# Performance work log

Hardware: AMD Instinct MI355X
Metric: run time of the kernel (lower is better)

The kernel has to match this reference:

```python
import jax, jax.numpy as jnp
import numpy as np
import math

D_MODEL = 512
NHEAD = 8
N_LAYERS = 3
D_FF = 2048
INPUT_DIM = 128
NUM_CLASSES = 64
FACTOR = 5


def setup_inputs() -> dict:
    key = jax.random.key(0)
    ks = jax.random.split(key, 24)
    s = 0.02
    d, f, nl = D_MODEL, D_FF, N_LAYERS
    inp = {
        "x": jax.random.normal(ks[0], (4, 1024, INPUT_DIM), dtype=jnp.float32),
        "W_emb": jax.random.normal(ks[1], (INPUT_DIM, d), dtype=jnp.float32) * s,
        "b_emb": jnp.zeros((d,), jnp.float32),
        "Wq": jax.random.normal(ks[2], (nl, d, d), dtype=jnp.float32) * s,
        "bq": jnp.zeros((nl, d), jnp.float32),
        "Wk": jax.random.normal(ks[3], (nl, d, d), dtype=jnp.float32) * s,
        "bk": jnp.zeros((nl, d), jnp.float32),
        "Wv": jax.random.normal(ks[4], (nl, d, d), dtype=jnp.float32) * s,
        "bv": jnp.zeros((nl, d), jnp.float32),
        "Wo": jax.random.normal(ks[5], (nl, d, d), dtype=jnp.float32) * s,
        "bo": jnp.zeros((nl, d), jnp.float32),
        "ln1_g": jnp.ones((nl, d), jnp.float32),
        "ln1_b": jnp.zeros((nl, d), jnp.float32),
        "W1": jax.random.normal(ks[6], (nl, d, f), dtype=jnp.float32) * s,
        "b1": jnp.zeros((nl, f), jnp.float32),
        "W2": jax.random.normal(ks[7], (nl, f, d), dtype=jnp.float32) * s,
        "b2": jnp.zeros((nl, d), jnp.float32),
        "ln2_g": jnp.ones((nl, d), jnp.float32),
        "ln2_b": jnp.zeros((nl, d), jnp.float32),
        "W_dec": jax.random.normal(ks[8], (d, NUM_CLASSES), dtype=jnp.float32) * s,
        "b_dec": jnp.zeros((NUM_CLASSES,), jnp.float32),
    }
    return inp


def _layer_norm(x, g, b, eps=1e-5):
    m = jnp.mean(x, axis=-1, keepdims=True)
    v = jnp.var(x, axis=-1, keepdims=True)
    return (x - m) * jax.lax.rsqrt(v + eps) * g + b


def _pos_encoding(L, d):
    pos = jnp.arange(L, dtype=jnp.float32)[:, None]
    div = jnp.exp(jnp.arange(0, d, 2, dtype=jnp.float32) * (-math.log(10000.0) / d))
    pe = jnp.zeros((L, d), jnp.float32)
    pe = pe.at[:, 0::2].set(jnp.sin(pos * div))
    pe = pe.at[:, 1::2].set(jnp.cos(pos * div))
    return pe


def _prob_sparse_attn(x, Wq, bq, Wk, bk, Wv, bv, Wo, bo):
    B, L, d = x.shape
    H, dk = NHEAD, d // NHEAD
    u = min(L, int(FACTOR * math.log(L)) if L > 1 else L)
    Q = (x @ Wq + bq).reshape(B, L, H, dk).transpose(0, 2, 1, 3)  # bhld
    K = (x @ Wk + bk).reshape(B, L, H, dk).transpose(0, 2, 1, 3)
    V = (x @ Wv + bv).reshape(B, L, H, dk).transpose(0, 2, 1, 3)
    scores = jnp.einsum("bhld,bhmd->bhlm", Q, K) / math.sqrt(dk)  # [B,H,L,L]
    kth = jax.lax.top_k(scores, u)[0][..., -1:]  # kth-largest per row
    scores = jnp.where(scores < kth, -10000.0, scores)
    attn = jax.nn.softmax(scores, axis=-1)
    out = jnp.einsum("bhlm,bhmd->bhld", attn, V)
    out = out.transpose(0, 2, 1, 3).reshape(B, L, d)
    return out @ Wo + bo


def reference(x, W_emb, b_emb, Wq, bq, Wk, bk, Wv, bv, Wo, bo,
              ln1_g, ln1_b, W1, b1, W2, b2, ln2_g, ln2_b, W_dec, b_dec):
    B, L, _ = x.shape
    h = (x @ W_emb + b_emb) * math.sqrt(D_MODEL)
    h = h + _pos_encoding(L, D_MODEL)[None]
    for i in range(N_LAYERS):
        a = _prob_sparse_attn(h, Wq[i], bq[i], Wk[i], bk[i], Wv[i], bv[i], Wo[i], bo[i])
        h = _layer_norm(h + a, ln1_g[i], ln1_b[i])
        ff = jax.nn.relu(h @ W1[i] + b1[i]) @ W2[i] + b2[i]
        h = _layer_norm(h + ff, ln2_g[i], ln2_b[i])
    return h @ W_dec + b_dec
```

## Files before the change

kernel.cpp:

```cpp
#include <hip/hip_runtime.h>
#include <math.h>

#define SEQ 1024
#define BATCH 4
#define DMODEL 512
#define NHEAD 8
#define DK 64
#define DFF 2048
#define U_TOP 34
#define ROWS (BATCH * SEQ)

typedef unsigned short ushort_t;
typedef __attribute__((ext_vector_type(8))) short short8;
typedef __attribute__((ext_vector_type(4))) float float4v;

__device__ inline ushort_t f2bf(float f) {
  unsigned u = __float_as_uint(f);
  unsigned r = u + 0x7fffu + ((u >> 16) & 1u);
  return (ushort_t)(r >> 16);
}
__device__ inline float bf2f(ushort_t u) {
  return __uint_as_float((unsigned)u << 16);
}
__device__ inline float keyinv(unsigned cand) {
  unsigned fb = (cand & 0x80000000u) ? (cand ^ 0x80000000u) : ~cand;
  return __uint_as_float(fb);
}

union H16 { _Float16 h; unsigned short u; };
__device__ inline unsigned short h2u(float f) {
  H16 t; t.h = (_Float16)f; return t.u;
}
__device__ inline float u2h(unsigned short u) {
  H16 t; t.u = u; return (float)t.h;
}
__device__ inline int mbcnt64(unsigned long long m) {
  int lo = __builtin_amdgcn_mbcnt_lo((unsigned)m, 0);
  return __builtin_amdgcn_mbcnt_hi((unsigned)(m >> 32), lo);
}

__device__ inline void glds16(const void* g, void* l) {
  __builtin_amdgcn_global_load_lds(
      (const __attribute__((address_space(1))) unsigned int*)g,
      (__attribute__((address_space(3))) unsigned int*)l, 16, 0, 0);
}

__device__ inline void bitonic64x2(float& a, float& b, int lane) {
#pragma unroll
  for (int k = 2; k <= 64; k <<= 1) {
#pragma unroll
    for (int j = k >> 1; j > 0; j >>= 1) {
      float pa = __shfl_xor(a, j);
      float pb = __shfl_xor(b, j);
      bool keepMin = (((lane & k) != 0) == ((lane & j) == 0));
      a = keepMin ? fminf(a, pa) : fmaxf(a, pa);
      b = keepMin ? fminf(b, pb) : fmaxf(b, pb);
    }
  }
}

template <int RELU, int SPLIT>
__global__ __launch_bounds__(256) void gemm128(
    const ushort_t* __restrict__ A, const short* __restrict__ Bt,
    const float* __restrict__ b0, const float* __restrict__ b1,
    const float* __restrict__ b2, ushort_t* __restrict__ Cout,
    int K, int N, int zCstride) {
  __shared__ short As[128 * 32];
  __shared__ short Bs[128 * 32];

  const int tid = threadIdx.x;
  const int lane = tid & 63, w = tid >> 6;
  const int wm = w >> 1, wn = w & 1;
  const int quad = lane >> 4, r16 = lane & 15;
  const int bm = blockIdx.y * 128, bn = blockIdx.x * 128;

  const int srow = lane >> 2, skseg = lane & 3;
  const ushort_t* Ag0 = A + (size_t)(bm + w * 16 + srow) * K + skseg * 8;
  const ushort_t* Ag1 = Ag0 + (size_t)64 * K;
  const short* Bg0 = Bt + (size_t)(bn + w * 16 + srow) * K + skseg * 8;
  const short* Bg1 = Bg0 + (size_t)64 * K;
  short* lA0 = As + (w * 16) * 32;
  short* lA1 = As + (64 + w * 16) * 32;
  short* lB0 = Bs + (w * 16) * 32;
  short* lB1 = Bs + (64 + w * 16) * 32;

  float4v acc[4][4];
#pragma unroll
  for (int m = 0; m < 4; ++m)
#pragma unroll
    for (int n = 0; n < 4; ++n) acc[m][n] = (float4v){0.f, 0.f, 0.f, 0.f};

  for (int k0 = 0; k0 < K; k0 += 32) {
    __syncthreads();
    glds16(Ag0 + k0, lA0);
    glds16(Ag1 + k0, lA1);
    glds16(Bg0 + k0, lB0);
    glds16(Bg1 + k0, lB1);
    __syncthreads();

    short8 af[4], bfr[4];
#pragma unroll
    for (int m = 0; m < 4; ++m)
      af[m] = *(const short8*)&As[(wm * 64 + m * 16 + r16) * 32 + quad * 8];
#pragma unroll
    for (int n = 0; n < 4; ++n)
      bfr[n] = *(const short8*)&Bs[(wn * 64 + n * 16 + r16) * 32 + quad * 8];
#pragma unroll
    for (int m = 0; m < 4; ++m)
#pragma unroll
      for (int n = 0; n < 4; ++n)
        acc[m][n] = __builtin_amdgcn_mfma_f32_16x16x32_bf16(af[m], bfr[n],
                                                            acc[m][n], 0, 0, 0);
  }

  const int z = SPLIT ? (bn >> 9) : 0;
  const float* bias = (z == 0) ? b0 : (z == 1 ? b1 : b2);
  const int cbase = SPLIT ? (bn & 511) : bn;
  const int strideN = SPLIT ? 512 : N;
  ushort_t* C = Cout + (SPLIT ? (size_t)z * zCstride : (size_t)0);

  float bias_n[4];
#pragma unroll
  for (int n = 0; n < 4; ++n)
    bias_n[n] = bias[cbase + wn * 64 + n * 16 + r16];

#pragma unroll
  for (int m = 0; m < 4; ++m) {
#pragma unroll
    for (int n = 0; n < 4; ++n) {
      int col = cbase + wn * 64 + n * 16 + r16;
#pragma unroll
      for (int reg = 0; reg < 4; ++reg) {
        int row = bm + wm * 64 + m * 16 + quad * 4 + reg;
        float v = acc[m][n][reg] + bias_n[n];
        if (RELU) v = fmaxf(v, 0.f);
        C[(size_t)row * strideN + col] = f2bf(v);
      }
    }
  }
}

__global__ __launch_bounds__(256) void gemm128sk(
    const ushort_t* __restrict__ A, const short* __restrict__ Bt,
    const float* __restrict__ bias, ushort_t* __restrict__ pout,
    int K, int Ks) {
  __shared__ short As[128 * 32];
  __shared__ short Bs[128 * 32];

  const int tid = threadIdx.x;
  const int lane = tid & 63, w = tid >> 6;
  const int wm = w >> 1, wn = w & 1;
  const int quad = lane >> 4, r16 = lane & 15;
  const int bm = blockIdx.y * 128, bn = blockIdx.x * 128;
  const int z = blockIdx.z;
  const int koff = z * Ks;

  const int srow = lane >> 2, skseg = lane & 3;
  const ushort_t* Ag0 =
      A + (size_t)(bm + w * 16 + srow) * K + skseg * 8 + koff;
  const ushort_t* Ag1 = Ag0 + (size_t)64 * K;
  const short* Bg0 = Bt + (size_t)(bn + w * 16 + srow) * K + skseg * 8 + koff;
  const short* Bg1 = Bg0 + (size_t)64 * K;
  short* lA0 = As + (w * 16) * 32;
  short* lA1 = As + (64 + w * 16) * 32;
  short* lB0 = Bs + (w * 16) * 32;
  short* lB1 = Bs + (64 + w * 16) * 32;

  float4v acc[4][4];
#pragma unroll
  for (int m = 0; m < 4; ++m)
#pragma unroll
    for (int n = 0; n < 4; ++n) acc[m][n] = (float4v){0.f, 0.f, 0.f, 0.f};

  for (int k0 = 0; k0 < Ks; k0 += 32) {
    __syncthreads();
    glds16(Ag0 + k0, lA0);
    glds16(Ag1 + k0, lA1);
    glds16(Bg0 + k0, lB0);
    glds16(Bg1 + k0, lB1);
    __syncthreads();

    short8 af[4], bfr[4];
#pragma unroll
    for (int m = 0; m < 4; ++m)
      af[m] = *(const short8*)&As[(wm * 64 + m * 16 + r16) * 32 + quad * 8];
#pragma unroll
    for (int n = 0; n < 4; ++n)
      bfr[n] = *(const short8*)&Bs[(wn * 64 + n * 16 + r16) * 32 + quad * 8];
#pragma unroll
    for (int m = 0; m < 4; ++m)
#pragma unroll
      for (int n = 0; n < 4; ++n)
        acc[m][n] = __builtin_amdgcn_mfma_f32_16x16x32_bf16(af[m], bfr[n],
                                                            acc[m][n], 0, 0, 0);
  }

  ushort_t* P = pout + (size_t)z * 2097152;
  float bias_n[4];
#pragma unroll
  for (int n = 0; n < 4; ++n)
    bias_n[n] = (z == 0) ? bias[bn + wn * 64 + n * 16 + r16] : 0.f;

#pragma unroll
  for (int m = 0; m < 4; ++m) {
#pragma unroll
    for (int n = 0; n < 4; ++n) {
      int col = bn + wn * 64 + n * 16 + r16;
#pragma unroll
      for (int reg = 0; reg < 4; ++reg) {
        int row = bm + wm * 64 + m * 16 + quad * 4 + reg;
        float v = acc[m][n][reg] + bias_n[n];
        P[(size_t)row * 512 + col] = f2bf(v);
      }
    }
  }
}

template <int RELU, int OUTBF16, int EPI, int ADDC>
__global__ __launch_bounds__(256) void gemm64(
    const ushort_t* __restrict__ A, const short* __restrict__ Bt,
    const float* __restrict__ bias, void* __restrict__ Cout,
    const ushort_t* __restrict__ Cadd, int K, int N) {
  __shared__ short As[64 * 32];
  __shared__ short Bs[64 * 32];

  const int tid = threadIdx.x;
  const int lane = tid & 63, w = tid >> 6;
  const int wm = w >> 1, wn = w & 1;
  const int quad = lane >> 4, r16 = lane & 15;
  const int bm = blockIdx.y * 64, bn = blockIdx.x * 64;

  const int srow = tid >> 2, skseg = tid & 3;
  const ushort_t* Ag = A + (size_t)(bm + srow) * K + skseg * 8;
  const short* Bg = Bt + (size_t)(bn + srow) * K + skseg * 8;
  short* lA = As + w * 512;
  short* lB = Bs + w * 512;

  float4v acc[2][2];
#pragma unroll
  for (int m = 0; m < 2; ++m)
#pragma unroll
    for (int n = 0; n < 2; ++n) acc[m][n] = (float4v){0.f, 0.f, 0.f, 0.f};

  for (int k0 = 0; k0 < K; k0 += 32) {
    __syncthreads();
    glds16(Ag + k0, lA);
    glds16(Bg + k0, lB);
    __syncthreads();

    short8 af[2], bfr[2];
#pragma unroll
    for (int m = 0; m < 2; ++m)
      af[m] = *(const short8*)&As[(wm * 32 + m * 16 + r16) * 32 + quad * 8];
#pragma unroll
    for (int n = 0; n < 2; ++n)
      bfr[n] = *(const short8*)&Bs[(wn * 32 + n * 16 + r16) * 32 + quad * 8];
#pragma unroll
    for (int m = 0; m < 2; ++m)
#pragma unroll
      for (int n = 0; n < 2; ++n)
        acc[m][n] = __builtin_amdgcn_mfma_f32_16x16x32_bf16(af[m], bfr[n],
                                                            acc[m][n], 0, 0, 0);
  }

  const float pe_c = (float)(-9.210340371976184 / 512.0);
  const float sqrtd = 22.62741699796952f;

  float bias_n[2];
#pragma unroll
  for (int n = 0; n < 2; ++n) bias_n[n] = bias[bn + wn * 32 + n * 16 + r16];

#pragma unroll
  for (int m = 0; m < 2; ++m) {
#pragma unroll
    for (int n = 0; n < 2; ++n) {
      int col = bn + wn * 32 + n * 16 + r16;
#pragma unroll
      for (int reg = 0; reg < 4; ++reg) {
        int row = bm + wm * 32 + m * 16 + quad * 4 + reg;
        float v = acc[m][n][reg] + bias_n[n];
        if (RELU) v = fmaxf(v, 0.f);
        if (EPI == 2) {
          int pos = row & (SEQ - 1);
          float e = __expf((float)(col & ~1) * pe_c);
          float arg = (float)pos * e;
          v = v * sqrtd + ((col & 1) ? __cosf(arg) : __sinf(arg));
        }
        if (ADDC) v += bf2f(Cadd[(size_t)row * N + col]);
        if (OUTBF16) {
          ((ushort_t*)Cout)[(size_t)row * N + col] = f2bf(v);
        } else {
          ((float*)Cout)[(size_t)row * N + col] = v;
        }
      }
    }
  }
}

__global__ __launch_bounds__(256) void convert_all(
    const float* __restrict__ Wq, const float* __restrict__ Wk,
    const float* __restrict__ Wv, const float* __restrict__ Wo,
    const float* __restrict__ W1, const float* __restrict__ W2,
    const float* __restrict__ W_emb, const float* __restrict__ W_dec,
    short* __restrict__ wt) {
  __shared__ float t[32][33];
  int id = blockIdx.x;
  const float* src;
  short* dst;
  int K, N, tk, tn;
  if (id < 9216) {
    int lay = id / 3072, r = id % 3072;
    short* wl = wt + (size_t)lay * 3145728;
    const size_t wsz = 512 * 512;
    if (r < 1024) {
      int wi = r >> 8, tile = r & 255;
      const float* base = (wi == 0) ? Wq : (wi == 1) ? Wk : (wi == 2) ? Wv : Wo;
      src = base + lay * wsz;
      dst = wl + wi * 262144;
      K = 512; N = 512; tk = tile >> 4; tn = tile & 15;
    } else if (r < 2048) {
      int tile = r - 1024;
      src = W1 + (size_t)lay * 512 * 2048;
      dst = wl + 1048576;
      K = 512; N = 2048; tk = tile >> 6; tn = tile & 63;
    } else {
      int tile = r - 2048;
      src = W2 + (size_t)lay * 2048 * 512;
      dst = wl + 2097152;
      K = 2048; N = 512; tk = tile >> 4; tn = tile & 15;
    }
  } else {
    int r = id - 9216;
    if (r < 64) {
      src = W_emb; dst = wt + 9437184; K = 128; N = 512; tk = r >> 4; tn = r & 15;
    } else {
      r -= 64;
      src = W_dec; dst = wt + 9502720; K = 512; N = 64; tk = r >> 1; tn = r & 1;
    }
  }
  const int k0 = tk * 32, n0 = tn * 32;
  const int tx = threadIdx.x, ty = threadIdx.y;
#pragma unroll
  for (int i = 0; i < 4; ++i) {
    int r = ty + i * 8;
    t[r][tx] = src[(size_t)(k0 + r) * N + n0 + tx];
  }
  __syncthreads();
#pragma unroll
  for (int i = 0; i < 4; ++i) {
    int r = ty + i * 8;
    dst[(size_t)(n0 + r) * K + k0 + tx] = (short)f2bf(t[tx][r]);
  }
}

__global__ __launch_bounds__(256) void f32_to_bf16_kernel(
    const float* __restrict__ src, ushort_t* __restrict__ dst) {
  int i = blockIdx.x * blockDim.x + threadIdx.x;
  float4 v = ((const float4*)src)[i];
  ushort4 o;
  o.x = f2bf(v.x); o.y = f2bf(v.y); o.z = f2bf(v.z); o.w = f2bf(v.w);
  ((ushort4*)dst)[i] = o;
}

__global__ __launch_bounds__(256) void ln_red_kernel(
    const ushort_t* __restrict__ pa, const ushort_t* __restrict__ pb,
    const float* __restrict__ g, const float* __restrict__ bb,
    ushort_t* __restrict__ hb) {
  const int row = blockIdx.x * 4 + (threadIdx.x >> 6);
  const int lane = threadIdx.x & 63;
  const size_t base = (size_t)row * DMODEL + lane * 8;
  uint4 ra = *(const uint4*)(pa + base);
  uint4 rb = *(const uint4*)(pb + base);
  uint4 rh = *(const uint4*)(hb + base);
  unsigned aa[4] = {ra.x, ra.y, ra.z, ra.w};
  unsigned ab[4] = {rb.x, rb.y, rb.z, rb.w};
  unsigned ah[4] = {rh.x, rh.y, rh.z, rh.w};
  float v[8];
#pragma unroll
  for (int k = 0; k < 4; ++k) {
    v[2 * k] = bf2f((ushort_t)(aa[k] & 0xffff)) +
               bf2f((ushort_t)(ab[k] & 0xffff)) +
               bf2f((ushort_t)(ah[k] & 0xffff));
    v[2 * k + 1] = bf2f((ushort_t)(aa[k] >> 16)) +
                   bf2f((ushort_t)(ab[k] >> 16)) +
                   bf2f((ushort_t)(ah[k] >> 16));
  }
  float sum = 0.f, sq = 0.f;
#pragma unroll
  for (int k = 0; k < 8; ++k) { sum += v[k]; sq += v[k] * v[k]; }
#pragma unroll
  for (int off = 32; off; off >>= 1) {
    sum += __shfl_xor(sum, off);
    sq += __shfl_xor(sq, off);
  }
  float mean = sum * (1.f / 512.f);
  float var = fmaxf(sq * (1.f / 512.f) - mean * mean, 0.f);
  float rstd = 1.f / sqrtf(var + 1e-5f);
  float4 g0 = *(const float4*)(g + lane * 8);
  float4 g1 = *(const float4*)(g + lane * 8 + 4);
  float4 c0 = *(const float4*)(bb + lane * 8);
  float4 c1 = *(const float4*)(bb + lane * 8 + 4);
  float gg[8] = {g0.x, g0.y, g0.z, g0.w, g1.x, g1.y, g1.z, g1.w};
  float cc[8] = {c0.x, c0.y, c0.z, c0.w, c1.x, c1.y, c1.z, c1.w};
  uint4 out;
  unsigned* op = (unsigned*)&out;
#pragma unroll
  for (int k = 0; k < 4; ++k) {
    float y0 = (v[2 * k] - mean) * rstd * gg[2 * k] + cc[2 * k];
    float y1 = (v[2 * k + 1] - mean) * rstd * gg[2 * k + 1] + cc[2 * k + 1];
    op[k] = (unsigned)f2bf(y0) | ((unsigned)f2bf(y1) << 16);
  }
  *(uint4*)(hb + base) = out;
}

#define SST 1048

__global__ __launch_bounds__(512, 8) void attn_kernel(
    const ushort_t* __restrict__ Qb, const ushort_t* __restrict__ Kb,
    const ushort_t* __restrict__ Vb, ushort_t* __restrict__ Ob) {
  __shared__ _Float16 s16[16 * SST];
  __shared__ unsigned plist[16][64];

  const int tid = threadIdx.x;
  const int q0 = blockIdx.x * 16;
  const int h = blockIdx.y;
  const int b = blockIdx.z;
  const int w = tid >> 6;
  const int lane = tid & 63;
  const int quad = lane >> 4, r16 = lane & 15;

  {
    const int j0 = w * 128;
    const ushort_t* qrow =
        Qb + (size_t)(b * SEQ + q0 + r16) * DMODEL + h * DK + quad * 8;
    short8 aq0 = *(const short8*)qrow;
    short8 aq1 = *(const short8*)(qrow + 32);

#pragma unroll
    for (int nt = 0; nt < 8; ++nt) {
      const ushort_t* krow =
          Kb + (size_t)(b * SEQ + j0 + nt * 16 + r16) * DMODEL + h * DK +
          quad * 8;
      short8 bk0 = *(const short8*)krow;
      short8 bk1 = *(const short8*)(krow + 32);
      float4v a = (float4v){0.f, 0.f, 0.f, 0.f};
      a = __builtin_amdgcn_mfma_f32_16x16x32_bf16(aq0, bk0, a, 0, 0, 0);
      a = __builtin_amdgcn_mfma_f32_16x16x32_bf16(aq1, bk1, a, 0, 0, 0);
#pragma unroll
      for (int reg = 0; reg < 4; ++reg)
        s16[(quad * 4 + reg) * SST + j0 + nt * 16 + r16] =
            (_Float16)(a[reg] * 0.125f);
    }
  }
  __syncthreads();

  {
    const int qa = w, qb2 = w + 8;
    const _Float16* sa = &s16[qa * SST];
    const _Float16* sb = &s16[qb2 * SST];

    float la = -1e30f, lb = -1e30f;
#pragma unroll
    for (int i = 0; i < 16; ++i) {
      la = fmaxf(la, (float)sa[lane + 64 * i]);
      lb = fmaxf(lb, (float)sb[lane + 64 * i]);
    }

    float sva = la, svb = lb;
    bitonic64x2(sva, svb, lane);
    const float mxa = __shfl(sva, 0), mxb = __shfl(svb, 0);
    const float fTa = __shfl(sva, 33), fTb = __shfl(svb, 33);

    int ca = 0, cb = 0;
#pragma unroll
    for (int i = 0; i < 16; ++i) {
      float va = (float)sa[lane + 64 * i];
      float vb = (float)sb[lane + 64 * i];
      bool ka = va >= fTa, kb = vb >= fTb;
      unsigned long long ma = __ballot(ka);
      unsigned long long mb = __ballot(kb);
      if (ka) {
        int p = ca + mbcnt64(ma);
        if (p < 64)
          plist[qa][p] = ((unsigned)(lane + 64 * i) << 16) |
                         h2u(__expf(va - mxa));
      }
      if (kb) {
        int p = cb + mbcnt64(mb);
        if (p < 64)
          plist[qb2][p] = ((unsigned)(lane + 64 * i) << 16) |
                          h2u(__expf(vb - mxb));
      }
      ca += (int)__popcll(ma);
      cb += (int)__popcll(mb);
    }

    if (__builtin_expect(ca > 64, 0)) {
      unsigned ans = 0u;
      int cge = ca;
      bool ex = false;
      for (int bit = 31; bit >= 0 && cge > 64 && !ex; --bit) {
        unsigned cand = ans | (1u << bit);
        float fc = keyinv(cand);
        int c = 0;
#pragma unroll
        for (int i = 0; i < 16; ++i)
          c += (int)__popcll(__ballot((float)sa[lane + 64 * i] >= fc));
        if (c >= U_TOP) { ans = cand; cge = c; ex = (c == U_TOP); }
      }
      float fa2 = keyinv(ans);
      int cc = 0;
#pragma unroll
      for (int i = 0; i < 16; ++i) {
        float va = (float)sa[lane + 64 * i];
        bool ka = va >= fa2;
        unsigned long long ma = __ballot(ka);
        if (ka) {
          int p = cc + mbcnt64(ma);
          if (p < 64)
            plist[qa][p] = ((unsigned)(lane + 64 * i) << 16) |
                           h2u(__expf(va - mxa));
        }
        cc += (int)__popcll(ma);
      }
      ca = cc;
    }
    if (__builtin_expect(cb > 64, 0)) {
      unsigned ans = 0u;
      int cge = cb;
      bool ex = false;
      for (int bit = 31; bit >= 0 && cge > 64 && !ex; --bit) {
        unsigned cand = ans | (1u << bit);
        float fc = keyinv(cand);
        int c = 0;
#pragma unroll
        for (int i = 0; i < 16; ++i)
          c += (int)__popcll(__ballot((float)sb[lane + 64 * i] >= fc));
        if (c >= U_TOP) { ans = cand; cge = c; ex = (c == U_TOP); }
      }
      float fb2 = keyinv(ans);
      int cc = 0;
#pragma unroll
      for (int i = 0; i < 16; ++i) {
        float vb = (float)sb[lane + 64 * i];
        bool kb = vb >= fb2;
        unsigned long long mb = __ballot(kb);
        if (kb) {
          int p = cc + mbcnt64(mb);
          if (p < 64)
            plist[qb2][p] = ((unsigned)(lane + 64 * i) << 16) |
                            h2u(__expf(vb - mxb));
        }
        cc += (int)__popcll(mb);
      }
      cb = cc;
    }
    ca = ca > 64 ? 64 : ca;
    cb = cb > 64 ? 64 : cb;

    unsigned pua = (lane < ca) ? plist[qa][lane] : 0u;
    unsigned pub = (lane < cb) ? plist[qb2][lane] : 0u;
    float ea = u2h((unsigned short)(pua & 0xffffu));
    float eb = u2h((unsigned short)(pub & 0xffffu));

    float s2a = ea, s2b = eb;
    bitonic64x2(s2a, s2b, lane);
    const float tha = __shfl(s2a, 33), thb = __shfl(s2b, 33);

    bool keepa = ea >= tha, keepb = eb >= thb;
    unsigned long long kma = __ballot(keepa);
    unsigned long long kmb = __ballot(keepb);
    int na = (int)__popcll(kma), nb = (int)__popcll(kmb);
    float za = keepa ? ea : 0.f, zb = keepb ? eb : 0.f;
#pragma unroll
    for (int off = 32; off; off >>= 1) {
      za += __shfl_xor(za, off);
      zb += __shfl_xor(zb, off);
    }
    int posa = mbcnt64(kma), posb = mbcnt64(kmb);
    if (keepa) plist[qa][posa] = pua;
    if (keepb) plist[qb2][posb] = pub;

    const ushort_t* vbase = Vb + (size_t)b * SEQ * DMODEL + h * DK;
    float oa = 0.f, ob = 0.f;
    int nmax = na > nb ? na : nb;
    for (int i = 0; i < nmax; i += 2) {
      unsigned ua0 = (i < na) ? plist[qa][i] : 0u;
      unsigned ua1 = (i + 1 < na) ? plist[qa][i + 1] : 0u;
      unsigned ub0 = (i < nb) ? plist[qb2][i] : 0u;
      unsigned ub1 = (i + 1 < nb) ? plist[qb2][i + 1] : 0u;
      float pa0 = bf2f(vbase[(size_t)(ua0 >> 16) * DMODEL + lane]);
      float pa1 = bf2f(vbase[(size_t)(ua1 >> 16) * DMODEL + lane]);
      float pb0 = bf2f(vbase[(size_t)(ub0 >> 16) * DMODEL + lane]);
      float pb1 = bf2f(vbase[(size_t)(ub1 >> 16) * DMODEL + lane]);
      oa += u2h((unsigned short)(ua0 & 0xffffu)) * pa0 +
            u2h((unsigned short)(ua1 & 0xffffu)) * pa1;
      ob += u2h((unsigned short)(ub0 & 0xffffu)) * pb0 +
            u2h((unsigned short)(ub1 & 0xffffu)) * pb1;
    }
    oa /= za;
    ob /= zb;
    Ob[(size_t)(b * SEQ + q0 + qa) * DMODEL + h * DK + lane] = f2bf(oa);
    Ob[(size_t)(b * SEQ + q0 + qb2) * DMODEL + h * DK + lane] = f2bf(ob);
  }
}

extern "C" void kernel_launch(void* const* d_in, const int* in_sizes, int n_in,
                              void* d_out, int out_size, void* d_ws,
                              size_t ws_size, hipStream_t stream) {
  const float* x = (const float*)d_in[0];
  const float* W_emb = (const float*)d_in[1];
  const float* b_emb = (const float*)d_in[2];
  const float* Wq = (const float*)d_in[3];
  const float* bq = (const float*)d_in[4];
  const float* Wk = (const float*)d_in[5];
  const float* bk = (const float*)d_in[6];
  const float* Wv = (const float*)d_in[7];
  const float* bv = (const float*)d_in[8];
  const float* Wo = (const float*)d_in[9];
  const float* bo = (const float*)d_in[10];
  const float* ln1_g = (const float*)d_in[11];
  const float* ln1_b = (const float*)d_in[12];
  const float* W1 = (const float*)d_in[13];
  const float* b1 = (const float*)d_in[14];
  const float* W2 = (const float*)d_in[15];
  const float* b2 = (const float*)d_in[16];
  const float* ln2_g = (const float*)d_in[17];
  const float* ln2_b = (const float*)d_in[18];
  const float* W_dec = (const float*)d_in[19];
  const float* b_dec = (const float*)d_in[20];

  char* wsb = (char*)d_ws;
  ushort_t* qkv = (ushort_t*)wsb;
  ushort_t* ffh = (ushort_t*)wsb;
  ushort_t* wop = (ushort_t*)wsb;
  ushort_t* ao = (ushort_t*)(wsb + ((size_t)16 << 20));
  ushort_t* xb = (ushort_t*)(wsb + ((size_t)16 << 20));
  ushort_t* ffp = (ushort_t*)(wsb + ((size_t)16 << 20));
  ushort_t* hb = (ushort_t*)(wsb + ((size_t)24 << 20));
  short* wt = (short*)(wsb + ((size_t)28 << 20));
  short* wembT = wt + 9437184;
  short* wdecT = wt + 9502720;

  f32_to_bf16_kernel<<<dim3(512), 256, 0, stream>>>(x, xb);
  convert_all<<<dim3(9312), dim3(32, 8), 0, stream>>>(Wq, Wk, Wv, Wo, W1, W2,
                                                      W_emb, W_dec, wt);
  gemm64<0, 1, 2, 0><<<dim3(8, 64), 256, 0, stream>>>(
      xb, wembT, b_emb, (void*)hb, nullptr, 128, 512);

  for (int i = 0; i < 3; ++i) {
    short* wtL = wt + (size_t)i * 3145728;

    gemm128<0, 1><<<dim3(12, 32), 256, 0, stream>>>(
        hb, wtL, bq + i * DMODEL, bk + i * DMODEL, bv + i * DMODEL, qkv, 512,
        512, 2097152);

    attn_kernel<<<dim3(SEQ / 16, NHEAD, BATCH), dim3(512), 0, stream>>>(
        qkv, qkv + 2097152, qkv + 4194304, ao);

    gemm128sk<<<dim3(4, 32, 2), 256, 0, stream>>>(
        ao, wtL + 786432, bo + i * DMODEL, wop, 512, 256);
    ln_red_kernel<<<dim3(ROWS / 4), 256, 0, stream>>>(
        wop, wop + 2097152, ln1_g + i * DMODEL, ln1_b + i * DMODEL, hb);

    gemm128<1, 0><<<dim3(16, 32), 256, 0, stream>>>(
        hb, wtL + 1048576, b1 + i * DFF, nullptr, nullptr, ffh, 512, 2048, 0);
    gemm128sk<<<dim3(4, 32, 2), 256, 0, stream>>>(
        ffh, wtL + 2097152, b2 + i * DMODEL, ffp, 2048, 1024);
    ln_red_kernel<<<dim3(ROWS / 4), 256, 0, stream>>>(
        ffp, ffp + 2097152, ln2_g + i * DMODEL, ln2_b + i * DMODEL, hb);
  }

  gemm64<0, 0, 0, 0><<<dim3(1, 64), 256, 0, stream>>>(
      hb, wdecT, b_dec, d_out, nullptr, 512, 64);
}
```

Before: 558.1 us.

## Remap blocks per XCD for L2 locality and defer exp in sparse attention

Both GEMM kernels now remap the linear block id so that each XCD handles a contiguous band of row tiles. The attention kernel likewise groups each XCD's blocks onto the same (batch, head) pairs, so K/V and A tiles get more reuse in each XCD's L2. In attention, scores are read from LDS as packed 32-bit pairs held in registers instead of being re-read per pass. The exp is now computed only for the kept top-k candidates rather than for every candidate above the first threshold. The remapping assumes grid dimensions divisible by 8 and a fixed 64x8x4 attention grid.

```diff
diff --git a/kernel.cpp b/kernel.cpp
--- a/kernel.cpp
+++ b/kernel.cpp
@@ -34,6 +34,8 @@
 __device__ inline float u2h(unsigned short u) {
   H16 t; t.u = u; return (float)t.h;
 }
+__device__ inline float lo16(unsigned u) { return u2h((unsigned short)(u & 0xffffu)); }
+__device__ inline float hi16(unsigned u) { return u2h((unsigned short)(u >> 16)); }
 __device__ inline int mbcnt64(unsigned long long m) {
   int lo = __builtin_amdgcn_mbcnt_lo((unsigned)m, 0);
   return __builtin_amdgcn_mbcnt_hi((unsigned)(m >> 32), lo);
@@ -72,7 +74,13 @@
   const int lane = tid & 63, w = tid >> 6;
   const int wm = w >> 1, wn = w & 1;
   const int quad = lane >> 4, r16 = lane & 15;
-  const int bm = blockIdx.y * 128, bn = blockIdx.x * 128;
+
+  const int id = blockIdx.y * gridDim.x + blockIdx.x;
+  const int xcd = id & 7;
+  const int loc = id >> 3;
+  const int rpx = gridDim.y >> 3;
+  const int bm = (xcd * rpx + (loc % rpx)) * 128;
+  const int bn = (loc / rpx) * 128;
 
   const int srow = lane >> 2, skseg = lane & 3;
   const ushort_t* Ag0 = A + (size_t)(bm + w * 16 + srow) * K + skseg * 8;
@@ -151,7 +159,13 @@
   const int lane = tid & 63, w = tid >> 6;
   const int wm = w >> 1, wn = w & 1;
   const int quad = lane >> 4, r16 = lane & 15;
-  const int bm = blockIdx.y * 128, bn = blockIdx.x * 128;
+
+  const int id = blockIdx.y * gridDim.x + blockIdx.x;
+  const int xcd = id & 7;
+  const int loc = id >> 3;
+  const int rpx = gridDim.y >> 3;
+  const int bm = (xcd * rpx + (loc % rpx)) * 128;
+  const int bn = (loc / rpx) * 128;
   const int z = blockIdx.z;
   const int koff = z * Ks;
 
@@ -422,9 +436,14 @@
   __shared__ unsigned plist[16][64];
 
   const int tid = threadIdx.x;
-  const int q0 = blockIdx.x * 16;
-  const int h = blockIdx.y;
-  const int b = blockIdx.z;
+  const int id = blockIdx.x + 64 * (blockIdx.y + 8 * blockIdx.z);
+  const int xcd = id & 7;
+  const int loc = id >> 3;
+  const int bh = xcd * 4 + (loc & 3);
+  const int q0 = (loc >> 2) * 16;
+  const int b = bh >> 3;
+  const int h = bh & 7;
+
   const int w = tid >> 6;
   const int lane = tid & 63;
   const int quad = lane >> 4, r16 = lane & 15;
@@ -458,12 +477,21 @@
     const int qa = w, qb2 = w + 8;
     const _Float16* sa = &s16[qa * SST];
     const _Float16* sb = &s16[qb2 * SST];
+    const unsigned* sa32 = (const unsigned*)sa;
+    const unsigned* sb32 = (const unsigned*)sb;
+
+    unsigned pk_a[8], pk_b[8];
+#pragma unroll
+    for (int i = 0; i < 8; ++i) {
+      pk_a[i] = sa32[lane + 64 * i];
+      pk_b[i] = sb32[lane + 64 * i];
+    }
 
     float la = -1e30f, lb = -1e30f;
 #pragma unroll
-    for (int i = 0; i < 16; ++i) {
-      la = fmaxf(la, (float)sa[lane + 64 * i]);
-      lb = fmaxf(lb, (float)sb[lane + 64 * i]);
+    for (int i = 0; i < 8; ++i) {
+      la = fmaxf(la, fmaxf(lo16(pk_a[i]), hi16(pk_a[i])));
+      lb = fmaxf(lb, fmaxf(lo16(pk_b[i]), hi16(pk_b[i])));
     }
 
     float sva = la, svb = lb;
@@ -474,22 +502,19 @@
     int ca = 0, cb = 0;
 #pragma unroll
     for (int i = 0; i < 16; ++i) {
-      float va = (float)sa[lane + 64 * i];
-      float vb = (float)sb[lane + 64 * i];
+      float va = (i & 1) ? hi16(pk_a[i >> 1]) : lo16(pk_a[i >> 1]);
+      float vb = (i & 1) ? hi16(pk_b[i >> 1]) : lo16(pk_b[i >> 1]);
+      int j = 2 * lane + (i & 1) + 128 * (i >> 1);
       bool ka = va >= fTa, kb = vb >= fTb;
       unsigned long long ma = __ballot(ka);
       unsigned long long mb = __ballot(kb);
       if (ka) {
         int p = ca + mbcnt64(ma);
-        if (p < 64)
-          plist[qa][p] = ((unsigned)(lane + 64 * i) << 16) |
-                         h2u(__expf(va - mxa));
+        if (p < 64) plist[qa][p] = ((unsigned)j << 16) | h2u(va);
       }
       if (kb) {
         int p = cb + mbcnt64(mb);
-        if (p < 64)
-          plist[qb2][p] = ((unsigned)(lane + 64 * i) << 16) |
-                          h2u(__expf(vb - mxb));
+        if (p < 64) plist[qb2][p] = ((unsigned)j << 16) | h2u(vb);
       }
       ca += (int)__popcll(ma);
       cb += (int)__popcll(mb);
@@ -518,8 +543,7 @@
         if (ka) {
           int p = cc + mbcnt64(ma);
           if (p < 64)
-            plist[qa][p] = ((unsigned)(lane + 64 * i) << 16) |
-                           h2u(__expf(va - mxa));
+            plist[qa][p] = ((unsigned)(lane + 64 * i) << 16) | h2u(va);
         }
         cc += (int)__popcll(ma);
       }
@@ -548,8 +572,7 @@
         if (kb) {
           int p = cc + mbcnt64(mb);
           if (p < 64)
-            plist[qb2][p] = ((unsigned)(lane + 64 * i) << 16) |
-                            h2u(__expf(vb - mxb));
+            plist[qb2][p] = ((unsigned)(lane + 64 * i) << 16) | h2u(vb);
         }
         cc += (int)__popcll(mb);
       }
@@ -560,26 +583,28 @@
 
     unsigned pua = (lane < ca) ? plist[qa][lane] : 0u;
     unsigned pub = (lane < cb) ? plist[qb2][lane] : 0u;
-    float ea = u2h((unsigned short)(pua & 0xffffu));
-    float eb = u2h((unsigned short)(pub & 0xffffu));
-
-    float s2a = ea, s2b = eb;
+    float cfa = (lane < ca) ? u2h((unsigned short)(pua & 0xffffu)) : -3.4e38f;
+    float cfb = (lane < cb) ? u2h((unsigned short)(pub & 0xffffu)) : -3.4e38f;
+
+    float s2a = cfa, s2b = cfb;
     bitonic64x2(s2a, s2b, lane);
     const float tha = __shfl(s2a, 33), thb = __shfl(s2b, 33);
 
-    bool keepa = ea >= tha, keepb = eb >= thb;
+    bool keepa = cfa >= tha, keepb = cfb >= thb;
     unsigned long long kma = __ballot(keepa);
     unsigned long long kmb = __ballot(keepb);
     int na = (int)__popcll(kma), nb = (int)__popcll(kmb);
-    float za = keepa ? ea : 0.f, zb = keepb ? eb : 0.f;
+    float ea = keepa ? __expf(cfa - mxa) : 0.f;
+    float eb = keepb ? __expf(cfb - mxb) : 0.f;
+    float za = ea, zb = eb;
 #pragma unroll
     for (int off = 32; off; off >>= 1) {
       za += __shfl_xor(za, off);
       zb += __shfl_xor(zb, off);
     }
     int posa = mbcnt64(kma), posb = mbcnt64(kmb);
-    if (keepa) plist[qa][posa] = pua;
-    if (keepb) plist[qb2][posb] = pub;
+    if (keepa) plist[qa][posa] = (pua & 0xffff0000u) | h2u(ea);
+    if (keepb) plist[qb2][posb] = (pub & 0xffff0000u) | h2u(eb);
 
     const ushort_t* vbase = Vb + (size_t)b * SEQ * DMODEL + h * DK;
     float oa = 0.f, ob = 0.f;
```

Result: no change. 553.2 us (-0.9%).
